# Kernel optimization log

Hardware: AMD Instinct MI355X
Metric: run time of the kernel (lower is better)

The kernel has to match this reference:

```python
import jax, jax.numpy as jnp
import numpy as np

H = 8          # num_heads
WIN = 256      # window_size (even); half-window = 128
NEG = -1e30    # stand-in for -inf that keeps softmax grad finite


def setup_inputs() -> dict:
    key = jax.random.key(0)
    ks = jax.random.split(key, 6)
    B, S, D, E = 2, 2048, 512, 512
    x = jax.random.normal(ks[0], (B, S, D), dtype=jnp.float32)
    padding_mask = jax.random.randint(ks[1], (B, S), 0, 2, dtype=jnp.int32)
    Wqkv = jax.random.normal(ks[2], (3 * E, D), dtype=jnp.float32) * 0.02
    bqkv = jnp.zeros((3 * E,), dtype=jnp.float32)
    Wo = jax.random.normal(ks[3], (E, E), dtype=jnp.float32) * 0.02
    bo = jnp.zeros((E,), dtype=jnp.float32)
    return {"x": x, "padding_mask": padding_mask, "Wqkv": Wqkv, "bqkv": bqkv,
            "Wo": Wo, "bo": bo}


def reference(x, padding_mask, Wqkv, bqkv, Wo, bo):
    B, S, _ = x.shape
    E = Wo.shape[0]
    Dh = E // H
    # qkv projection -> [B, H, S, 3*Dh]
    qkv = (x @ Wqkv.T + bqkv).reshape(B, S, H, 3 * Dh).transpose(0, 2, 1, 3)
    q, k, v = jnp.split(qkv, 3, axis=-1)
    # full S x S scores (original materializes [B,H,S,S]); scale by sqrt(head_dim)
    scores = jnp.einsum('bhsd,bhtd->bhst', q, k) / jnp.sqrt(jnp.float32(Dh))
    # sliding-window band: |i - j| <= window_size // 2
    i = jnp.arange(S)[:, None]
    j = jnp.arange(S)[None, :]
    band = jnp.abs(i - j) <= (WIN // 2)               # [S, S]
    # padding: entry valid only if both row and col tokens are non-pad
    pad = padding_mask.astype(bool)                    # [B, S]
    valid = band[None, None] & pad[:, None, None, :] & pad[:, None, :, None]
    scores = jnp.where(valid, scores, NEG)
    A = jax.nn.softmax(scores, axis=-1)
    # rows with no valid entry -> nan_to_num(., 0) in original -> zeros here
    row_valid = jnp.any(valid, axis=-1, keepdims=True)
    A = jnp.where(row_valid, A, 0.0)
    Y = jnp.einsum('bhst,bhtd->bhsd', A, v)            # [B,H,S,Dh]
    Y = Y.transpose(0, 2, 1, 3).reshape(B, S, E)
    return Y @ Wo.T + bo
```

## Files before the change

### kernel.cpp

```cpp
#include <hip/hip_runtime.h>

#define NH   8
#define SEQ  2048
#define DIM  512
#define EMB  512
#define DH   64
#define HALF 128
#define QT   16
#define KW   272
#define SCS  276

typedef __attribute__((ext_vector_type(8))) short short8;
typedef __attribute__((ext_vector_type(4))) float f32x4;

__device__ __forceinline__ unsigned short f2bf(float f) {
    unsigned int u = __float_as_uint(f);
    return (unsigned short)((u + 0x7fffu + ((u >> 16) & 1u)) >> 16);
}

__device__ __forceinline__ unsigned cvtpk(float lo, float hi) {
    unsigned r;
    asm("v_cvt_pk_bf16_f32 %0, %1, %2" : "=v"(r) : "v"(lo), "v"(hi));
    return r;
}

__device__ __forceinline__ void gload_lds16(const void* g, void* l) {
    __builtin_amdgcn_global_load_lds((__attribute__((address_space(1))) void*)g,
                                     (__attribute__((address_space(3))) void*)l,
                                     16, 0, 0);
}

__global__ __launch_bounds__(256)
void gemm_qkv(const float* __restrict__ A, const float* __restrict__ B,
              const float* __restrict__ bias, unsigned short* __restrict__ qkvh,
              unsigned short* __restrict__ vT) {
    constexpr int BM = 128, BN = 64, BK = 64;
    __shared__ unsigned short As[2][BM * BK];
    __shared__ unsigned short Bs[2][BN * BK];
    const int bid = blockIdx.x;
    const int wg = (bid & 7) * 96 + (bid >> 3);
    const int bm = (wg / 24) * BM, bn = (wg % 24) * BN;
    const int t = threadIdx.x, lane = t & 63, wid = t >> 6;
    const int wr = wid >> 1, wc = wid & 1;
    const int lr = lane & 15, lg = lane >> 4;

    f32x4 acc[4][2];
    #pragma unroll
    for (int m = 0; m < 4; ++m)
        #pragma unroll
        for (int n = 0; n < 2; ++n)
            acc[m][n] = (f32x4){0.f, 0.f, 0.f, 0.f};

    float4 rA[4][2], rB[2][2];
    auto loadA = [&](int kt) {
        #pragma unroll
        for (int i = 0; i < 4; ++i) {
            const int c = t + 256 * i, r = c >> 3, c8 = c & 7;
            const float4* s = (const float4*)(A + (size_t)(bm + r) * DIM + kt + c8 * 8);
            rA[i][0] = s[0]; rA[i][1] = s[1];
        }
    };
    auto loadB = [&](int kt) {
        #pragma unroll
        for (int i = 0; i < 2; ++i) {
            const int c = t + 256 * i, r = c >> 3, c8 = c & 7;
            const float4* s = (const float4*)(B + (size_t)(bn + r) * DIM + kt + c8 * 8);
            rB[i][0] = s[0]; rB[i][1] = s[1];
        }
    };

    loadA(0); loadB(0);
    for (int it = 0; it < 8; ++it) {
        const int cur = it & 1;
        #pragma unroll
        for (int i = 0; i < 4; ++i) {
            const int c = t + 256 * i, r = c >> 3, c8 = c & 7;
            const uint4 pk = make_uint4(cvtpk(rA[i][0].x, rA[i][0].y), cvtpk(rA[i][0].z, rA[i][0].w),
                                        cvtpk(rA[i][1].x, rA[i][1].y), cvtpk(rA[i][1].z, rA[i][1].w));
            *(uint4*)&As[cur][r * 64 + ((c8 ^ (r & 7)) << 3)] = pk;
        }
        #pragma unroll
        for (int i = 0; i < 2; ++i) {
            const int c = t + 256 * i, r = c >> 3, c8 = c & 7;
            const uint4 pk = make_uint4(cvtpk(rB[i][0].x, rB[i][0].y), cvtpk(rB[i][0].z, rB[i][0].w),
                                        cvtpk(rB[i][1].x, rB[i][1].y), cvtpk(rB[i][1].z, rB[i][1].w));
            *(uint4*)&Bs[cur][r * 64 + ((c8 ^ (r & 7)) << 3)] = pk;
        }
        __syncthreads();
        if (it < 7) { loadA((it + 1) * BK); loadB((it + 1) * BK); }

        short8 af[2][4], bf[2][2];
        #pragma unroll
        for (int kk = 0; kk < 2; ++kk) {
            #pragma unroll
            for (int m = 0; m < 4; ++m) {
                const int row = wr * 64 + m * 16 + lr;
                af[kk][m] = *(const short8*)&As[cur][row * 64 + (((kk * 4 + lg) ^ (row & 7)) << 3)];
            }
            #pragma unroll
            for (int n = 0; n < 2; ++n) {
                const int row = wc * 32 + n * 16 + lr;
                bf[kk][n] = *(const short8*)&Bs[cur][row * 64 + (((kk * 4 + lg) ^ (row & 7)) << 3)];
            }
        }
        #pragma unroll
        for (int kk = 0; kk < 2; ++kk)
            #pragma unroll
            for (int m = 0; m < 4; ++m)
                #pragma unroll
                for (int n = 0; n < 2; ++n)
                    acc[m][n] = __builtin_amdgcn_mfma_f32_16x16x32_bf16(af[kk][m], bf[kk][n], acc[m][n], 0, 0, 0);
    }
    __syncthreads();

    unsigned short* Tr = &As[0][0];
    #pragma unroll
    for (int n = 0; n < 2; ++n) {
        const int cl = wc * 32 + n * 16 + lr;
        const float bv = bias[bn + cl];
        #pragma unroll
        for (int m = 0; m < 4; ++m)
            #pragma unroll
            for (int r = 0; r < 4; ++r)
                Tr[(wr * 64 + m * 16 + lg * 4 + r) * 72 + cl] = f2bf(acc[m][n][r] + bv);
    }
    __syncthreads();

    const int h = bn / 192, ty = (bn >> 6) % 3;
    const int bb = bm >> 11, s0 = bm & 2047;
    if (ty < 2) {
        unsigned short* plane = qkvh + (((size_t)(bb * NH + h) * 3 + ty) * SEQ) * DH;
        const int s = t >> 1, hf = (t & 1) * 32;
        unsigned short* dst = plane + (size_t)(s0 + s) * DH + hf;
        #pragma unroll
        for (int k8 = 0; k8 < 4; ++k8)
            *(short8*)&dst[k8 * 8] = *(const short8*)&Tr[s * 72 + hf + k8 * 8];
    } else {
        const int d = t >> 2, pp = t & 3;
        unsigned short* vrow = vT + ((size_t)(bb * NH + h) * DH + d) * SEQ + s0 + pp * 32;
        #pragma unroll
        for (int k8 = 0; k8 < 4; ++k8) {
            alignas(16) unsigned short tmp[8];
            #pragma unroll
            for (int k = 0; k < 8; ++k) tmp[k] = Tr[(pp * 32 + k8 * 8 + k) * 72 + d];
            *(short8*)&vrow[k8 * 8] = *(short8*)tmp;
        }
    }
}

__global__ __launch_bounds__(256)
void attn_mfma(const unsigned short* __restrict__ qkvh,
               const unsigned short* __restrict__ vT,
               const int* __restrict__ pad,
               unsigned short* __restrict__ Yb) {
    const int bid = blockIdx.x;
    const int wg = (bid & 7) * 256 + (bid >> 3);
    const int bh = wg >> 7, qt = wg & 127;
    const int b = bh >> 3, h = bh & 7;
    const int i0 = qt * QT, kb = i0 - HALF;
    const int t = threadIdx.x, lane = t & 63, w = t >> 6;
    const int lr = lane & 15, lg = lane >> 4;

    __shared__ float Sc[QT * SCS];

    const unsigned short* Qg = qkvh + ((size_t)bh * 3 + 0) * SEQ * DH;
    const unsigned short* Kg = qkvh + ((size_t)bh * 3 + 1) * SEQ * DH;
    const unsigned short* vTg = vT + (size_t)bh * DH * SEQ;
    const int* padb = pad + b * SEQ;

    short8 qf[2];
    #pragma unroll
    for (int kk = 0; kk < 2; ++kk)
        qf[kk] = *(const short8*)&Qg[(size_t)(i0 + lr) * DH + kk * 32 + lg * 8];

    const int k0 = w * 16;
    #pragma unroll
    for (int c = 0; c < 5; ++c) {
        const int nc = (c < 4) ? 64 : 16;
        if (k0 < nc) {
            const int jl = c * 64 + k0 + lr;
            const int j = kb + jl;
            const int jc = j < 0 ? 0 : (j > SEQ - 1 ? SEQ - 1 : j);
            const int kv = (j >= 0 && j < SEQ) ? padb[j] : 0;
            f32x4 a0 = (f32x4){0.f, 0.f, 0.f, 0.f};
            #pragma unroll
            for (int kk = 0; kk < 2; ++kk) {
                const short8 bfr = *(const short8*)&Kg[(size_t)jc * DH + kk * 32 + lg * 8];
                a0 = __builtin_amdgcn_mfma_f32_16x16x32_bf16(qf[kk], bfr, a0, 0, 0, 0);
            }
            #pragma unroll
            for (int r = 0; r < 4; ++r) {
                const int q0 = lg * 4 + r;
                const bool ok = kv && (jl >= q0) && (jl <= q0 + 2 * HALF);
                Sc[q0 * SCS + jl] = ok ? a0[r] * 0.125f : -1e30f;
            }
        }
    }
    __syncthreads();

    for (int r = w; r < QT; r += 4) {
        float* row = &Sc[r * SCS];
        unsigned short* prow = (unsigned short*)row;
        if (!padb[i0 + r]) {
            #pragma unroll
            for (int u = 0; u < 5; ++u) {
                const int jl = lane + 64 * u;
                if (jl < KW) prow[jl] = 0;
            }
            if (lane >= 16 && lane < 32) prow[256 + lane] = 0;
            continue;
        }
        float v[5];
        float mx = -1e30f;
        #pragma unroll
        for (int u = 0; u < 5; ++u) {
            const int jl = lane + 64 * u;
            v[u] = (jl < KW) ? row[jl] : -1e30f;
            mx = fmaxf(mx, v[u]);
        }
        #pragma unroll
        for (int off = 32; off; off >>= 1) mx = fmaxf(mx, __shfl_xor(mx, off));
        float s = 0.f;
        #pragma unroll
        for (int u = 0; u < 5; ++u) { v[u] = __expf(v[u] - mx); s += v[u]; }
        #pragma unroll
        for (int off = 32; off; off >>= 1) s += __shfl_xor(s, off);
        const float inv = 1.f / s;
        asm volatile("" ::: "memory");
        #pragma unroll
        for (int u = 0; u < 5; ++u) {
            const int jl = lane + 64 * u;
            if (jl < KW) prow[jl] = f2bf(v[u] * inv);
        }
        if (lane >= 16 && lane < 32) prow[256 + lane] = 0;
    }
    __syncthreads();

    f32x4 o0 = (f32x4){0.f, 0.f, 0.f, 0.f};
    const unsigned short* PbU = (const unsigned short*)Sc;
    const int d0 = w * 16 + lr;
    #pragma unroll
    for (int c = 0; c < 5; ++c) {
        const int nkk = (c < 4) ? 2 : 1;
        #pragma unroll
        for (int kk = 0; kk < nkk; ++kk) {
            int j0 = kb + c * 64 + kk * 32 + lg * 8;
            j0 = j0 < 0 ? 0 : (j0 > SEQ - 8 ? SEQ - 8 : j0);
            const short8 vf = *(const short8*)&vTg[(size_t)d0 * SEQ + j0];
            const short8 pf = *(const short8*)&PbU[lr * (SCS * 2) + c * 64 + kk * 32 + lg * 8];
            o0 = __builtin_amdgcn_mfma_f32_16x16x32_bf16(pf, vf, o0, 0, 0, 0);
        }
    }

    #pragma unroll
    for (int r = 0; r < 4; ++r)
        Yb[(size_t)(b * SEQ + i0 + lg * 4 + r) * EMB + h * DH + d0] = f2bf(o0[r]);
}

__global__ __launch_bounds__(256)
void gemm_out(const unsigned short* __restrict__ A, const float* __restrict__ B,
              const float* __restrict__ bias, float* __restrict__ C) {
    constexpr int BM = 64, BN = 64, BK = 64;
    __shared__ unsigned short As[2][BM * BK];
    __shared__ unsigned short Bs[2][BN * BK];
    const int bid = blockIdx.x;
    const int wg = (bid & 7) * 64 + (bid >> 3);
    const int bm = (wg >> 3) * BM, bn = (wg & 7) * BN;
    const int t = threadIdx.x, lane = t & 63, wid = t >> 6;
    const int wr = wid >> 1, wc = wid & 1;
    const int lr = lane & 15, lg = lane >> 4;

    f32x4 acc[2][2];
    #pragma unroll
    for (int m = 0; m < 2; ++m)
        #pragma unroll
        for (int n = 0; n < 2; ++n)
            acc[m][n] = (f32x4){0.f, 0.f, 0.f, 0.f};

    float4 rB[2][2];
    auto gloadA = [&](int kt, int buf) {
        #pragma unroll
        for (int off = 0; off < BM * BK; off += 2048) {
            const int e = off + t * 8, r = e >> 6, c4 = (e & 63) >> 3;
            const int gc = (c4 ^ (r & 7)) << 3;
            gload_lds16(A + (size_t)(bm + r) * EMB + kt + gc, &As[buf][e]);
        }
    };
    auto loadB = [&](int kt) {
        #pragma unroll
        for (int i = 0; i < 2; ++i) {
            const int c = t + 256 * i, r = c >> 3, c8 = c & 7;
            const float4* s = (const float4*)(B + (size_t)(bn + r) * DIM + kt + c8 * 8);
            rB[i][0] = s[0]; rB[i][1] = s[1];
        }
    };

    gloadA(0, 0);
    loadB(0);
    for (int it = 0; it < 8; ++it) {
        const int cur = it & 1;
        #pragma unroll
        for (int i = 0; i < 2; ++i) {
            const int c = t + 256 * i, r = c >> 3, c8 = c & 7;
            const uint4 pk = make_uint4(cvtpk(rB[i][0].x, rB[i][0].y), cvtpk(rB[i][0].z, rB[i][0].w),
                                        cvtpk(rB[i][1].x, rB[i][1].y), cvtpk(rB[i][1].z, rB[i][1].w));
            *(uint4*)&Bs[cur][r * 64 + ((c8 ^ (r & 7)) << 3)] = pk;
        }
        __syncthreads();
        if (it < 7) { gloadA((it + 1) * BK, cur ^ 1); loadB((it + 1) * BK); }

        short8 af[2][2], bf[2][2];
        #pragma unroll
        for (int kk = 0; kk < 2; ++kk) {
            #pragma unroll
            for (int m = 0; m < 2; ++m) {
                const int row = wr * 32 + m * 16 + lr;
                af[kk][m] = *(const short8*)&As[cur][row * BK + (((kk * 4 + lg) ^ (row & 7)) << 3)];
            }
            #pragma unroll
            for (int n = 0; n < 2; ++n) {
                const int row = wc * 32 + n * 16 + lr;
                bf[kk][n] = *(const short8*)&Bs[cur][row * BK + (((kk * 4 + lg) ^ (row & 7)) << 3)];
            }
        }
        #pragma unroll
        for (int kk = 0; kk < 2; ++kk)
            #pragma unroll
            for (int m = 0; m < 2; ++m)
                #pragma unroll
                for (int n = 0; n < 2; ++n)
                    acc[m][n] = __builtin_amdgcn_mfma_f32_16x16x32_bf16(af[kk][m], bf[kk][n], acc[m][n], 0, 0, 0);
    }

    const int orow = bm + wr * 32 + lg * 4;
    const int oc0 = bn + wc * 32 + lr;
    #pragma unroll
    for (int m = 0; m < 2; ++m)
        #pragma unroll
        for (int n = 0; n < 2; ++n) {
            const int col = oc0 + n * 16;
            const float bv = bias[col];
            #pragma unroll
            for (int r = 0; r < 4; ++r)
                C[(size_t)(orow + m * 16 + r) * EMB + col] = acc[m][n][r] + bv;
        }
}

extern "C" void kernel_launch(void* const* d_in, const int* in_sizes, int n_in,
                              void* d_out, int out_size, void* d_ws, size_t ws_size,
                              hipStream_t stream) {
    const float* x    = (const float*)d_in[0];
    const int*   pad  = (const int*)d_in[1];
    const float* Wqkv = (const float*)d_in[2];
    const float* bqkv = (const float*)d_in[3];
    const float* Wo   = (const float*)d_in[4];
    const float* bo   = (const float*)d_in[5];
    float* out = (float*)d_out;

    char* p = (char*)d_ws;
    unsigned short* qkvh = (unsigned short*)p;
    unsigned short* vT   = (unsigned short*)(p + 12582912);
    unsigned short* Yb   = (unsigned short*)(p + 16777216);

    dim3 blk(256);
    gemm_qkv<<<dim3(768), blk, 0, stream>>>(x, Wqkv, bqkv, qkvh, vT);
    attn_mfma<<<dim3(2048), blk, 0, stream>>>(qkvh, vT, pad, Yb);
    gemm_out<<<dim3(512), blk, 0, stream>>>(Yb, Wo, bo, out);
}
```

Before: 56.99 us.

## Give each wave its own 16-query tile in attention, removing block barriers

The attention kernel now gives each of the four waves in a block an independent 16-row query tile (64 queries per block) with a private LDS score buffer. This replaces the old scheme where four waves cooperated on one 16-row tile and synchronized with __syncthreads. Each wave now computes all 17 key tiles and all four head-dim output tiles itself, and the grid shrinks from 2048 to 512 blocks. This removes block barriers and splits the launch more coarsely, at the cost of more work per wave and 4x the LDS per block, which may lower occupancy.

```diff
diff --git a/kernel.cpp b/kernel.cpp
--- a/kernel.cpp
+++ b/kernel.cpp
@@ -6,7 +6,7 @@
 #define EMB  512
 #define DH   64
 #define HALF 128
-#define QT   16
+#define QTB  64
 #define KW   272
 #define SCS  276
 
@@ -154,14 +154,16 @@
                const int* __restrict__ pad,
                unsigned short* __restrict__ Yb) {
     const int bid = blockIdx.x;
-    const int wg = (bid & 7) * 256 + (bid >> 3);
-    const int bh = wg >> 7, qt = wg & 127;
+    const int wg = (bid & 7) * 64 + (bid >> 3);
+    const int bh = wg >> 5, qt = wg & 31;
     const int b = bh >> 3, h = bh & 7;
-    const int i0 = qt * QT, kb = i0 - HALF;
     const int t = threadIdx.x, lane = t & 63, w = t >> 6;
     const int lr = lane & 15, lg = lane >> 4;
-
-    __shared__ float Sc[QT * SCS];
+    const int i0 = qt * QTB + w * 16;
+    const int kb = i0 - HALF;
+
+    __shared__ float ScAll[4][16 * SCS];
+    float* Sc = ScAll[w];
 
     const unsigned short* Qg = qkvh + ((size_t)bh * 3 + 0) * SEQ * DH;
     const unsigned short* Kg = qkvh + ((size_t)bh * 3 + 1) * SEQ * DH;
@@ -173,32 +175,28 @@
     for (int kk = 0; kk < 2; ++kk)
         qf[kk] = *(const short8*)&Qg[(size_t)(i0 + lr) * DH + kk * 32 + lg * 8];
 
-    const int k0 = w * 16;
-    #pragma unroll
-    for (int c = 0; c < 5; ++c) {
-        const int nc = (c < 4) ? 64 : 16;
-        if (k0 < nc) {
-            const int jl = c * 64 + k0 + lr;
-            const int j = kb + jl;
-            const int jc = j < 0 ? 0 : (j > SEQ - 1 ? SEQ - 1 : j);
-            const int kv = (j >= 0 && j < SEQ) ? padb[j] : 0;
-            f32x4 a0 = (f32x4){0.f, 0.f, 0.f, 0.f};
-            #pragma unroll
-            for (int kk = 0; kk < 2; ++kk) {
-                const short8 bfr = *(const short8*)&Kg[(size_t)jc * DH + kk * 32 + lg * 8];
-                a0 = __builtin_amdgcn_mfma_f32_16x16x32_bf16(qf[kk], bfr, a0, 0, 0, 0);
-            }
-            #pragma unroll
-            for (int r = 0; r < 4; ++r) {
-                const int q0 = lg * 4 + r;
-                const bool ok = kv && (jl >= q0) && (jl <= q0 + 2 * HALF);
-                Sc[q0 * SCS + jl] = ok ? a0[r] * 0.125f : -1e30f;
-            }
-        }
-    }
-    __syncthreads();
-
-    for (int r = w; r < QT; r += 4) {
+    #pragma unroll
+    for (int jt = 0; jt < 17; ++jt) {
+        const int jl = jt * 16 + lr;
+        const int j = kb + jl;
+        const int jc = j < 0 ? 0 : (j > SEQ - 1 ? SEQ - 1 : j);
+        const int kv = (j >= 0 && j < SEQ) ? padb[j] : 0;
+        f32x4 a0 = (f32x4){0.f, 0.f, 0.f, 0.f};
+        #pragma unroll
+        for (int kk = 0; kk < 2; ++kk) {
+            const short8 bfr = *(const short8*)&Kg[(size_t)jc * DH + kk * 32 + lg * 8];
+            a0 = __builtin_amdgcn_mfma_f32_16x16x32_bf16(qf[kk], bfr, a0, 0, 0, 0);
+        }
+        #pragma unroll
+        for (int r = 0; r < 4; ++r) {
+            const int q0 = lg * 4 + r;
+            const bool ok = kv && (jl >= q0) && (jl <= q0 + 2 * HALF);
+            Sc[q0 * SCS + jl] = ok ? a0[r] * 0.125f : -1e30f;
+        }
+    }
+    asm volatile("" ::: "memory");
+
+    for (int r = 0; r < 16; ++r) {
         float* row = &Sc[r * SCS];
         unsigned short* prow = (unsigned short*)row;
         if (!padb[i0 + r]) {
@@ -234,11 +232,12 @@
         }
         if (lane >= 16 && lane < 32) prow[256 + lane] = 0;
     }
-    __syncthreads();
-
-    f32x4 o0 = (f32x4){0.f, 0.f, 0.f, 0.f};
+    asm volatile("" ::: "memory");
+
+    f32x4 o[4];
+    #pragma unroll
+    for (int dt = 0; dt < 4; ++dt) o[dt] = (f32x4){0.f, 0.f, 0.f, 0.f};
     const unsigned short* PbU = (const unsigned short*)Sc;
-    const int d0 = w * 16 + lr;
     #pragma unroll
     for (int c = 0; c < 5; ++c) {
         const int nkk = (c < 4) ? 2 : 1;
@@ -246,15 +245,20 @@
         for (int kk = 0; kk < nkk; ++kk) {
             int j0 = kb + c * 64 + kk * 32 + lg * 8;
             j0 = j0 < 0 ? 0 : (j0 > SEQ - 8 ? SEQ - 8 : j0);
-            const short8 vf = *(const short8*)&vTg[(size_t)d0 * SEQ + j0];
             const short8 pf = *(const short8*)&PbU[lr * (SCS * 2) + c * 64 + kk * 32 + lg * 8];
-            o0 = __builtin_amdgcn_mfma_f32_16x16x32_bf16(pf, vf, o0, 0, 0, 0);
-        }
-    }
-
-    #pragma unroll
-    for (int r = 0; r < 4; ++r)
-        Yb[(size_t)(b * SEQ + i0 + lg * 4 + r) * EMB + h * DH + d0] = f2bf(o0[r]);
+            #pragma unroll
+            for (int dt = 0; dt < 4; ++dt) {
+                const short8 vf = *(const short8*)&vTg[(size_t)(dt * 16 + lr) * SEQ + j0];
+                o[dt] = __builtin_amdgcn_mfma_f32_16x16x32_bf16(pf, vf, o[dt], 0, 0, 0);
+            }
+        }
+    }
+
+    #pragma unroll
+    for (int dt = 0; dt < 4; ++dt)
+        #pragma unroll
+        for (int r = 0; r < 4; ++r)
+            Yb[(size_t)(b * SEQ + i0 + lg * 4 + r) * EMB + h * DH + dt * 16 + lr] = f2bf(o[dt][r]);
 }
 
 __global__ __launch_bounds__(256)
@@ -364,6 +368,6 @@
 
     dim3 blk(256);
     gemm_qkv<<<dim3(768), blk, 0, stream>>>(x, Wqkv, bqkv, qkvh, vT);
-    attn_mfma<<<dim3(2048), blk, 0, stream>>>(qkvh, vT, pad, Yb);
+    attn_mfma<<<dim3(512), blk, 0, stream>>>(qkvh, vT, pad, Yb);
     gemm_out<<<dim3(512), blk, 0, stream>>>(Yb, Wo, bo, out);
 }
```

After: 61.09 us. 7.2% more time.
